# Kernel optimization log

Measured on AMD Instinct MI355X. Metric: run time of the kernel, lower is better.

Reference implementation:

```python
import jax, jax.numpy as jnp
import numpy as np

LEVELS = [(100, 128), (50, 64), (25, 32), (13, 16), (7, 8)]
B, C, S = 16, 80, 17064  # batch, class_num, sum(h*w)
GAMMA, ALPHA = 2.0, 0.25


def setup_inputs() -> dict:
    key = jax.random.key(0)
    ks = iter(jax.random.split(key, 40))
    inp = {}
    for i, (h, w) in enumerate(LEVELS):
        inp[f"cls_p{i}"] = jax.random.normal(next(ks), (B, C, h, w), dtype=jnp.float32)
        inp[f"cnt_p{i}"] = jax.random.normal(next(ks), (B, 1, h, w), dtype=jnp.float32)
        inp[f"reg_p{i}"] = jax.random.uniform(next(ks), (B, 4, h, w), dtype=jnp.float32) * 8.0 + 0.1
    keep = jax.random.uniform(next(ks), (B, S, 1)) > 0.7
    cnt_val = jax.random.uniform(next(ks), (B, S, 1), dtype=jnp.float32)
    inp["cnt_targets"] = jnp.where(keep, cnt_val, -1.0)
    inp["reg_targets"] = jax.random.uniform(next(ks), (B, S, 4), dtype=jnp.float32) * 8.0 + 0.1
    inp["cls_targets"] = jax.random.randint(next(ks), (B, S, 1), 0, 81, dtype=jnp.int64)
    return inp


def _flatten_levels(preds, c):
    # each pred [B,c,h,w] -> [B,h*w,c]; concat over levels -> [B,S,c]
    return jnp.concatenate(
        [p.transpose(0, 2, 3, 1).reshape(p.shape[0], -1, c) for p in preds], axis=1)


def _fcos_loss(cls_ps, cnt_ps, reg_ps, cls_t, cnt_t, reg_t):
    mask = (cnt_t > -1.0)[..., 0]                       # [B,S] bool positive mask
    num_pos = jnp.clip(jnp.sum(mask, axis=1), 1).astype(jnp.float32)  # [B]

    # ---- focal cls loss (over ALL locations, as in the original) ----
    cls = _flatten_levels(cls_ps, C)                    # [B,S,C]
    onehot = (jnp.arange(1, C + 1)[None, None, :] == cls_t).astype(jnp.float32)
    p = jax.nn.sigmoid(cls)
    p_t = onehot * p + (1.0 - onehot) * (1.0 - p)
    alpha_f = onehot * ALPHA + (1.0 - onehot) * (1.0 - ALPHA)
    focal = -alpha_f * (1.0 - p_t) ** GAMMA * jnp.log(p_t)
    cls_loss = jnp.mean(jnp.sum(focal, axis=(1, 2)) / num_pos)

    # ---- centerness BCE-with-logits, masked sum ----
    cnt = _flatten_levels(cnt_ps, 1)[..., 0]            # [B,S]
    t = cnt_t[..., 0]
    bce = jnp.maximum(cnt, 0.0) - cnt * t + jnp.log1p(jnp.exp(-jnp.abs(cnt)))
    cnt_loss = jnp.mean(jnp.sum(bce * mask, axis=1) / num_pos)

    # ---- GIoU reg loss, masked sum ----
    reg = _flatten_levels(reg_ps, 4)                    # [B,S,4] ltrb offsets
    lt_min = jnp.minimum(reg[..., :2], reg_t[..., :2])
    rb_min = jnp.minimum(reg[..., 2:], reg_t[..., 2:])
    wh_min = jnp.clip(rb_min + lt_min, 0.0)
    overlap = wh_min[..., 0] * wh_min[..., 1]
    area1 = (reg[..., 2] + reg[..., 0]) * (reg[..., 3] + reg[..., 1])
    area2 = (reg_t[..., 2] + reg_t[..., 0]) * (reg_t[..., 3] + reg_t[..., 1])
    union = area1 + area2 - overlap
    iou = overlap / union
    lt_max = jnp.maximum(reg[..., :2], reg_t[..., :2])
    rb_max = jnp.maximum(reg[..., 2:], reg_t[..., 2:])
    wh_max = jnp.clip(rb_max + lt_max, 0.0)
    g_area = wh_max[..., 0] * wh_max[..., 1]
    giou = iou - (g_area - union) / jnp.clip(g_area, 1e-10)
    reg_loss = jnp.mean(jnp.sum((1.0 - giou) * mask, axis=1) / num_pos)

    total = cls_loss + cnt_loss + reg_loss  # add_centerness=True
    return (cls_loss, cnt_loss, reg_loss, total)


def reference(cls_p0, cls_p1, cls_p2, cls_p3, cls_p4,
              cnt_p0, cnt_p1, cnt_p2, cnt_p3, cnt_p4,
              reg_p0, reg_p1, reg_p2, reg_p3, reg_p4,
              cnt_targets, reg_targets, cls_targets):
    return _fcos_loss([cls_p0, cls_p1, cls_p2, cls_p3, cls_p4],
                      [cnt_p0, cnt_p1, cnt_p2, cnt_p3, cnt_p4],
                      [reg_p0, reg_p1, reg_p2, reg_p3, reg_p4],
                      cls_targets, cnt_targets, reg_targets)
```

## Files before the change

### kernel.cpp

```cpp
#include <hip/hip_runtime.h>

#define S_TOTAL 17064
#define NB 16
#define NC 80
#define QPB 4266
#define NXQ 17

#define NA_BLOCKS 2064
#define SLOTS_PER_B 129
#define WSB 2064
#define NBXQ (NB * NXQ)

typedef float vfloat4 __attribute__((ext_vector_type(4)));

struct Ptrs {
    const float* cls[5];
    const float* cnt[5];
    const float* reg[5];
    const float* cnt_t;
    const float* reg_t;
    const int*   cls_t;
    float*       ws;
    float*       out;
};

__device__ __forceinline__ float focal_term(float x, bool o) {
    const float xs = o ? x : -x;
    const float af = o ? 0.25f : 0.75f;
    const float em = __expf(-xs);
    const float pt = 1.0f / (1.0f + em);
    const float q  = em * pt;
    return af * q * q * __logf(1.0f + em);
}

__device__ __forceinline__ float giou_term(float pl, float pt_, float pr, float pb,
                                           float tl, float tt, float tr, float tb) {
    const float overlap = fmaxf(fminf(pr, tr) + fminf(pl, tl), 0.0f) *
                          fmaxf(fminf(pb, tb) + fminf(pt_, tt), 0.0f);
    const float area1 = (pr + pl) * (pb + pt_);
    const float area2 = (tr + tl) * (tb + tt);
    const float uni = area1 + area2 - overlap;
    const float iou = overlap / uni;
    const float ga = fmaxf(fmaxf(pr, tr) + fmaxf(pl, tl), 0.0f) *
                     fmaxf(fmaxf(pb, tb) + fmaxf(pt_, tt), 0.0f);
    const float giou = iou - (ga - uni) / fmaxf(ga, 1e-10f);
    return 1.0f - giou;
}

__device__ __forceinline__ float bce_term(float x, float t) {
    return fmaxf(x, 0.0f) - x * t + __logf(1.0f + __expf(-fabsf(x)));
}

__global__ __launch_bounds__(256) void fcos_neg(Ptrs p) {
    const int bx = (int)blockIdx.x;

    int lvl, b, cnk, slot, CH, TOT;
    if (bx < 1536)      { lvl = 0; b = bx / 96;  cnk = bx - 96 * b;
                          slot = cnk;        CH = 2667; TOT = 256000; }
    else if (bx < 1920) { const int r = bx - 1536; lvl = 1; b = r / 24; cnk = r - 24 * b;
                          slot = 96 + cnk;   CH = 2667; TOT = 64000; }
    else if (bx < 2016) { const int r = bx - 1920; lvl = 2; b = r / 6;  cnk = r - 6 * b;
                          slot = 120 + cnk;  CH = 2667; TOT = 16000; }
    else if (bx < 2048) { const int r = bx - 2016; lvl = 3; b = r >> 1; cnk = r & 1;
                          slot = 126 + cnk;  CH = 2080; TOT = 4160; }
    else                { const int r = bx - 2048; lvl = 4; b = r;      cnk = 0;
                          slot = 128;        CH = 1120; TOT = 1120; }

    const vfloat4* bp = (const vfloat4*)(p.cls[lvl] + (size_t)b * 4 * TOT);
    const int i0   = cnk * CH;
    const int iend = min(i0 + CH, TOT);

    float acc = 0.f;
    #pragma unroll 2
    for (int i = i0 + (int)threadIdx.x; i < iend; i += 256) {
        const vfloat4 v = bp[i];
        acc += (focal_term(v.x, false) + focal_term(v.y, false)) +
               (focal_term(v.z, false) + focal_term(v.w, false));
    }

    #pragma unroll
    for (int d = 32; d; d >>= 1) acc += __shfl_down(acc, d);

    __shared__ float red[4];
    const int wave = threadIdx.x >> 6;
    if ((threadIdx.x & 63) == 0) red[wave] = acc;
    __syncthreads();
    if (threadIdx.x == 0)
        p.ws[b * SLOTS_PER_B + slot] = (red[0] + red[1]) + (red[2] + red[3]);
}

__global__ __launch_bounds__(256) void fcos_pos(Ptrs p) {
    const int bid = (int)blockIdx.x;
    const int b   = bid / NXQ;
    const int xq  = bid - b * NXQ;
    const int fq  = xq * 256 + (int)threadIdx.x;

    int lvl, qb, hw, off;
    if (fq < 3200)      { lvl = 0; qb = 0;    hw = 12800; off = 0;     }
    else if (fq < 4000) { lvl = 1; qb = 3200; hw = 3200;  off = 12800; }
    else if (fq < 4200) { lvl = 2; qb = 4000; hw = 800;   off = 16000; }
    else if (fq < 4252) { lvl = 3; qb = 4200; hw = 208;   off = 16800; }
    else                { lvl = 4; qb = 4252; hw = 56;    off = 17008; }
    const bool active = (fq < QPB);

    float corr = 0.f, acnt = 0.f, areg = 0.f, apos = 0.f;

    if (active) {
        const int s0  = (fq - qb) << 2;
        const int gs0 = b * S_TOTAL + off + s0;
        const int4 tq = *(const int4*)(p.cls_t + gs0);
        const float* cb = p.cls[lvl] + (size_t)(b * NC) * hw + s0;

        #pragma unroll
        for (int e = 0; e < 4; ++e) {
            const int ti = (e == 0) ? tq.x : (e == 1) ? tq.y : (e == 2) ? tq.z : tq.w;
            if (ti > 0) {
                const float x = cb[(size_t)(ti - 1) * hw + e];
                corr += focal_term(x, true) - focal_term(x, false);
            }
        }

        const float4 tC  = *(const float4*)(p.cnt_t + gs0);
        const float4 xc  = *(const float4*)(p.cnt[lvl] + (size_t)(b * hw + s0));
        const float m0 = (tC.x > -1.0f) ? 1.0f : 0.0f;
        const float m1 = (tC.y > -1.0f) ? 1.0f : 0.0f;
        const float m2 = (tC.z > -1.0f) ? 1.0f : 0.0f;
        const float m3 = (tC.w > -1.0f) ? 1.0f : 0.0f;
        apos = m0 + m1 + m2 + m3;
        acnt = bce_term(xc.x, tC.x) * m0 + bce_term(xc.y, tC.y) * m1 +
               bce_term(xc.z, tC.z) * m2 + bce_term(xc.w, tC.w) * m3;

        const float* rp  = p.reg[lvl] + (size_t)(b * 4 * hw + s0);
        const float4 pl  = *(const float4*)(rp);
        const float4 pt_ = *(const float4*)(rp + (size_t)hw);
        const float4 pr  = *(const float4*)(rp + (size_t)(2 * hw));
        const float4 pb  = *(const float4*)(rp + (size_t)(3 * hw));
        const float4 t0  = *(const float4*)(p.reg_t + (size_t)(gs0 + 0) * 4);
        const float4 t1  = *(const float4*)(p.reg_t + (size_t)(gs0 + 1) * 4);
        const float4 t2  = *(const float4*)(p.reg_t + (size_t)(gs0 + 2) * 4);
        const float4 t3  = *(const float4*)(p.reg_t + (size_t)(gs0 + 3) * 4);

        areg = giou_term(pl.x, pt_.x, pr.x, pb.x, t0.x, t0.y, t0.z, t0.w) * m0 +
               giou_term(pl.y, pt_.y, pr.y, pb.y, t1.x, t1.y, t1.z, t1.w) * m1 +
               giou_term(pl.z, pt_.z, pr.z, pb.z, t2.x, t2.y, t2.z, t2.w) * m2 +
               giou_term(pl.w, pt_.w, pr.w, pb.w, t3.x, t3.y, t3.z, t3.w) * m3;
    }

    #pragma unroll
    for (int d = 32; d; d >>= 1) {
        corr += __shfl_down(corr, d);
        acnt += __shfl_down(acnt, d);
        areg += __shfl_down(areg, d);
        apos += __shfl_down(apos, d);
    }

    __shared__ float red[4][4];
    const int wave = threadIdx.x >> 6;
    const int lane = threadIdx.x & 63;
    if (lane == 0) {
        red[0][wave] = corr; red[1][wave] = acnt;
        red[2][wave] = areg; red[3][wave] = apos;
    }
    __syncthreads();
    if (threadIdx.x == 0) {
        const int s = b * NXQ + xq;
        p.ws[WSB + 0 * NBXQ + s] = red[0][0] + red[0][1] + red[0][2] + red[0][3];
        p.ws[WSB + 1 * NBXQ + s] = red[1][0] + red[1][1] + red[1][2] + red[1][3];
        p.ws[WSB + 2 * NBXQ + s] = red[2][0] + red[2][1] + red[2][2] + red[2][3];
        p.ws[WSB + 3 * NBXQ + s] = red[3][0] + red[3][1] + red[3][2] + red[3][3];
    }
}

__global__ __launch_bounds__(256) void fcos_finalize(const float* __restrict__ ws,
                                                     float* __restrict__ out) {
    __shared__ float s[4][256];
    __shared__ float lb[3][NB];
    const int t = (int)threadIdx.x;
    const int b = t >> 4;
    const int k = t & 15;

    float qc = 0.f;
    for (int i = k; i < SLOTS_PER_B; i += 16) qc += ws[b * SLOTS_PER_B + i];
    float q1 = 0.f, q2 = 0.f, q3 = 0.f;
    for (int i = k; i < NXQ; i += 16) {
        const int sl = b * NXQ + i;
        qc += ws[WSB + 0 * NBXQ + sl];
        q1 += ws[WSB + 1 * NBXQ + sl];
        q2 += ws[WSB + 2 * NBXQ + sl];
        q3 += ws[WSB + 3 * NBXQ + sl];
    }
    s[0][t] = qc; s[1][t] = q1; s[2][t] = q2; s[3][t] = q3;
    __syncthreads();

    if (t < NB) {
        float cls = 0.f, cnt = 0.f, reg = 0.f, pos = 0.f;
        #pragma unroll
        for (int kk = 0; kk < 16; ++kk) {
            cls += s[0][t * 16 + kk];
            cnt += s[1][t * 16 + kk];
            reg += s[2][t * 16 + kk];
            pos += s[3][t * 16 + kk];
        }
        const float np = fmaxf(pos, 1.0f);
        lb[0][t] = cls / np;
        lb[1][t] = cnt / np;
        lb[2][t] = reg / np;
    }
    __syncthreads();

    if (t == 0) {
        float l0 = 0.f, l1 = 0.f, l2 = 0.f;
        #pragma unroll
        for (int bb = 0; bb < NB; ++bb) {
            l0 += lb[0][bb]; l1 += lb[1][bb]; l2 += lb[2][bb];
        }
        l0 *= (1.0f / NB); l1 *= (1.0f / NB); l2 *= (1.0f / NB);
        out[0] = l0;
        out[1] = l1;
        out[2] = l2;
        out[3] = l0 + l1 + l2;
    }
}

extern "C" void kernel_launch(void* const* d_in, const int* in_sizes, int n_in,
                              void* d_out, int out_size, void* d_ws, size_t ws_size,
                              hipStream_t stream) {
    Ptrs p;
    for (int i = 0; i < 5; ++i) {
        p.cls[i] = (const float*)d_in[3 * i + 0];
        p.cnt[i] = (const float*)d_in[3 * i + 1];
        p.reg[i] = (const float*)d_in[3 * i + 2];
    }
    p.cnt_t = (const float*)d_in[15];
    p.reg_t = (const float*)d_in[16];
    p.cls_t = (const int*)  d_in[17];
    p.ws    = (float*)d_ws;
    p.out   = (float*)d_out;

    fcos_neg<<<dim3(NA_BLOCKS), 256, 0, stream>>>(p);
    fcos_pos<<<dim3(NBXQ), 256, 0, stream>>>(p);
    fcos_finalize<<<dim3(1), 256, 0, stream>>>((const float*)d_ws, (float*)d_out);
}
```

Before: 161.3 us.

## Merge negative and positive passes into one kernel with per-element target labels

The separate negative-sweep and positive-correction kernels become a single launch that branches on block index. The cls sweep now reads the class-target row for each element and computes the exact focal term with the right one-hot flag, so the scattered gather-based correction is gone. One launch and one dependent global gather are removed, at the cost of extra int4 target loads and an integer division per vector in the hot loop, plus a templated loop structure.

After: 153.5 us. -4.9%, faster.

```diff
diff --git a/kernel.cpp b/kernel.cpp
--- a/kernel.cpp
+++ b/kernel.cpp
@@ -10,6 +10,7 @@
 #define SLOTS_PER_B 129
 #define WSB 2064
 #define NBXQ (NB * NXQ)
+#define TOTAL_GRID (NA_BLOCKS + NBXQ)
 
 typedef float vfloat4 __attribute__((ext_vector_type(4)));
 
@@ -51,123 +52,136 @@
     return fmaxf(x, 0.0f) - x * t + __logf(1.0f + __expf(-fabsf(x)));
 }
 
-__global__ __launch_bounds__(256) void fcos_neg(Ptrs p) {
+__device__ __forceinline__ float focal_quad(vfloat4 v, int4 t, int c1) {
+    return (focal_term(v.x, t.x == c1) + focal_term(v.y, t.y == c1)) +
+           (focal_term(v.z, t.z == c1) + focal_term(v.w, t.w == c1));
+}
+
+template <int HW4>
+__device__ __forceinline__ float sweep_cls(const vfloat4* __restrict__ bp,
+                                           const int* __restrict__ ct,
+                                           int u0, int stride) {
+    const int SPAN = NC * HW4;
+    float a0 = 0.f, a1 = 0.f;
+    int u = u0;
+    for (; u + stride < SPAN; u += 2 * stride) {
+        const int ub = u + stride;
+        const vfloat4 va = bp[u];
+        const vfloat4 vb = bp[ub];
+        const int ca = u / HW4;
+        const int cb = ub / HW4;
+        const int4 ta = *(const int4*)(ct + ((u  - ca * HW4) << 2));
+        const int4 tb = *(const int4*)(ct + ((ub - cb * HW4) << 2));
+        a0 += focal_quad(va, ta, ca + 1);
+        a1 += focal_quad(vb, tb, cb + 1);
+    }
+    if (u < SPAN) {
+        const vfloat4 v = bp[u];
+        const int c = u / HW4;
+        const int4 t = *(const int4*)(ct + ((u - c * HW4) << 2));
+        a0 += focal_quad(v, t, c + 1);
+    }
+    return a0 + a1;
+}
+
+__global__ __launch_bounds__(256) void fcos_main(Ptrs p) {
     const int bx = (int)blockIdx.x;
-
-    int lvl, b, cnk, slot, CH, TOT;
-    if (bx < 1536)      { lvl = 0; b = bx / 96;  cnk = bx - 96 * b;
-                          slot = cnk;        CH = 2667; TOT = 256000; }
-    else if (bx < 1920) { const int r = bx - 1536; lvl = 1; b = r / 24; cnk = r - 24 * b;
-                          slot = 96 + cnk;   CH = 2667; TOT = 64000; }
-    else if (bx < 2016) { const int r = bx - 1920; lvl = 2; b = r / 6;  cnk = r - 6 * b;
-                          slot = 120 + cnk;  CH = 2667; TOT = 16000; }
-    else if (bx < 2048) { const int r = bx - 2016; lvl = 3; b = r >> 1; cnk = r & 1;
-                          slot = 126 + cnk;  CH = 2080; TOT = 4160; }
-    else                { const int r = bx - 2048; lvl = 4; b = r;      cnk = 0;
-                          slot = 128;        CH = 1120; TOT = 1120; }
-
-    const vfloat4* bp = (const vfloat4*)(p.cls[lvl] + (size_t)b * 4 * TOT);
-    const int i0   = cnk * CH;
-    const int iend = min(i0 + CH, TOT);
-
-    float acc = 0.f;
-    #pragma unroll 2
-    for (int i = i0 + (int)threadIdx.x; i < iend; i += 256) {
-        const vfloat4 v = bp[i];
-        acc += (focal_term(v.x, false) + focal_term(v.y, false)) +
-               (focal_term(v.z, false) + focal_term(v.w, false));
-    }
-
-    #pragma unroll
-    for (int d = 32; d; d >>= 1) acc += __shfl_down(acc, d);
-
-    __shared__ float red[4];
-    const int wave = threadIdx.x >> 6;
-    if ((threadIdx.x & 63) == 0) red[wave] = acc;
-    __syncthreads();
-    if (threadIdx.x == 0)
-        p.ws[b * SLOTS_PER_B + slot] = (red[0] + red[1]) + (red[2] + red[3]);
-}
-
-__global__ __launch_bounds__(256) void fcos_pos(Ptrs p) {
-    const int bid = (int)blockIdx.x;
-    const int b   = bid / NXQ;
-    const int xq  = bid - b * NXQ;
-    const int fq  = xq * 256 + (int)threadIdx.x;
-
-    int lvl, qb, hw, off;
-    if (fq < 3200)      { lvl = 0; qb = 0;    hw = 12800; off = 0;     }
-    else if (fq < 4000) { lvl = 1; qb = 3200; hw = 3200;  off = 12800; }
-    else if (fq < 4200) { lvl = 2; qb = 4000; hw = 800;   off = 16000; }
-    else if (fq < 4252) { lvl = 3; qb = 4200; hw = 208;   off = 16800; }
-    else                { lvl = 4; qb = 4252; hw = 56;    off = 17008; }
-    const bool active = (fq < QPB);
-
-    float corr = 0.f, acnt = 0.f, areg = 0.f, apos = 0.f;
-
-    if (active) {
-        const int s0  = (fq - qb) << 2;
-        const int gs0 = b * S_TOTAL + off + s0;
-        const int4 tq = *(const int4*)(p.cls_t + gs0);
-        const float* cb = p.cls[lvl] + (size_t)(b * NC) * hw + s0;
-
-        #pragma unroll
-        for (int e = 0; e < 4; ++e) {
-            const int ti = (e == 0) ? tq.x : (e == 1) ? tq.y : (e == 2) ? tq.z : tq.w;
-            if (ti > 0) {
-                const float x = cb[(size_t)(ti - 1) * hw + e];
-                corr += focal_term(x, true) - focal_term(x, false);
-            }
-        }
-
-        const float4 tC  = *(const float4*)(p.cnt_t + gs0);
-        const float4 xc  = *(const float4*)(p.cnt[lvl] + (size_t)(b * hw + s0));
-        const float m0 = (tC.x > -1.0f) ? 1.0f : 0.0f;
-        const float m1 = (tC.y > -1.0f) ? 1.0f : 0.0f;
-        const float m2 = (tC.z > -1.0f) ? 1.0f : 0.0f;
-        const float m3 = (tC.w > -1.0f) ? 1.0f : 0.0f;
-        apos = m0 + m1 + m2 + m3;
-        acnt = bce_term(xc.x, tC.x) * m0 + bce_term(xc.y, tC.y) * m1 +
-               bce_term(xc.z, tC.z) * m2 + bce_term(xc.w, tC.w) * m3;
-
-        const float* rp  = p.reg[lvl] + (size_t)(b * 4 * hw + s0);
-        const float4 pl  = *(const float4*)(rp);
-        const float4 pt_ = *(const float4*)(rp + (size_t)hw);
-        const float4 pr  = *(const float4*)(rp + (size_t)(2 * hw));
-        const float4 pb  = *(const float4*)(rp + (size_t)(3 * hw));
-        const float4 t0  = *(const float4*)(p.reg_t + (size_t)(gs0 + 0) * 4);
-        const float4 t1  = *(const float4*)(p.reg_t + (size_t)(gs0 + 1) * 4);
-        const float4 t2  = *(const float4*)(p.reg_t + (size_t)(gs0 + 2) * 4);
-        const float4 t3  = *(const float4*)(p.reg_t + (size_t)(gs0 + 3) * 4);
-
-        areg = giou_term(pl.x, pt_.x, pr.x, pb.x, t0.x, t0.y, t0.z, t0.w) * m0 +
-               giou_term(pl.y, pt_.y, pr.y, pb.y, t1.x, t1.y, t1.z, t1.w) * m1 +
-               giou_term(pl.z, pt_.z, pr.z, pb.z, t2.x, t2.y, t2.z, t2.w) * m2 +
-               giou_term(pl.w, pt_.w, pr.w, pb.w, t3.x, t3.y, t3.z, t3.w) * m3;
-    }
-
-    #pragma unroll
-    for (int d = 32; d; d >>= 1) {
-        corr += __shfl_down(corr, d);
-        acnt += __shfl_down(acnt, d);
-        areg += __shfl_down(areg, d);
-        apos += __shfl_down(apos, d);
-    }
-
     __shared__ float red[4][4];
     const int wave = threadIdx.x >> 6;
     const int lane = threadIdx.x & 63;
-    if (lane == 0) {
-        red[0][wave] = corr; red[1][wave] = acnt;
-        red[2][wave] = areg; red[3][wave] = apos;
-    }
-    __syncthreads();
-    if (threadIdx.x == 0) {
-        const int s = b * NXQ + xq;
-        p.ws[WSB + 0 * NBXQ + s] = red[0][0] + red[0][1] + red[0][2] + red[0][3];
-        p.ws[WSB + 1 * NBXQ + s] = red[1][0] + red[1][1] + red[1][2] + red[1][3];
-        p.ws[WSB + 2 * NBXQ + s] = red[2][0] + red[2][1] + red[2][2] + red[2][3];
-        p.ws[WSB + 3 * NBXQ + s] = red[3][0] + red[3][1] + red[3][2] + red[3][3];
+
+    if (bx < NA_BLOCKS) {
+        int lvl, b, cnk, Kb, slot;
+        if (bx < 1536)      { lvl = 0; b = bx / 96;  cnk = bx - 96 * b;  Kb = 96; slot = cnk; }
+        else if (bx < 1920) { const int r = bx - 1536; lvl = 1; b = r / 24; cnk = r - 24 * b; Kb = 24; slot = 96 + cnk; }
+        else if (bx < 2016) { const int r = bx - 1920; lvl = 2; b = r / 6;  cnk = r - 6 * b;  Kb = 6;  slot = 120 + cnk; }
+        else if (bx < 2048) { const int r = bx - 2016; lvl = 3; b = r >> 1; cnk = r & 1;      Kb = 2;  slot = 126 + cnk; }
+        else                { lvl = 4; b = bx - 2048;  cnk = 0;            Kb = 1;            slot = 128; }
+
+        const int u0     = cnk * 256 + (int)threadIdx.x;
+        const int stride = Kb * 256;
+        float acc = 0.f;
+        switch (lvl) {
+            case 0: acc = sweep_cls<3200>((const vfloat4*)p.cls[0] + (size_t)b * (NC * 3200),
+                                          p.cls_t + b * S_TOTAL + 0,     u0, stride); break;
+            case 1: acc = sweep_cls<800>((const vfloat4*)p.cls[1] + (size_t)b * (NC * 800),
+                                          p.cls_t + b * S_TOTAL + 12800, u0, stride); break;
+            case 2: acc = sweep_cls<200>((const vfloat4*)p.cls[2] + (size_t)b * (NC * 200),
+                                          p.cls_t + b * S_TOTAL + 16000, u0, stride); break;
+            case 3: acc = sweep_cls<52>((const vfloat4*)p.cls[3] + (size_t)b * (NC * 52),
+                                          p.cls_t + b * S_TOTAL + 16800, u0, stride); break;
+            default: acc = sweep_cls<14>((const vfloat4*)p.cls[4] + (size_t)b * (NC * 14),
+                                          p.cls_t + b * S_TOTAL + 17008, u0, stride); break;
+        }
+
+        #pragma unroll
+        for (int d = 32; d; d >>= 1) acc += __shfl_down(acc, d);
+        if (lane == 0) red[0][wave] = acc;
+        __syncthreads();
+        if (threadIdx.x == 0)
+            p.ws[b * SLOTS_PER_B + slot] = (red[0][0] + red[0][1]) + (red[0][2] + red[0][3]);
+
+    } else {
+        const int bid = bx - NA_BLOCKS;
+        const int b   = bid / NXQ;
+        const int xq  = bid - b * NXQ;
+        const int fq  = xq * 256 + (int)threadIdx.x;
+
+        int lvl, qb, hw, off;
+        if (fq < 3200)      { lvl = 0; qb = 0;    hw = 12800; off = 0;     }
+        else if (fq < 4000) { lvl = 1; qb = 3200; hw = 3200;  off = 12800; }
+        else if (fq < 4200) { lvl = 2; qb = 4000; hw = 800;   off = 16000; }
+        else if (fq < 4252) { lvl = 3; qb = 4200; hw = 208;   off = 16800; }
+        else                { lvl = 4; qb = 4252; hw = 56;    off = 17008; }
+        const bool active = (fq < QPB);
+
+        float acnt = 0.f, areg = 0.f, apos = 0.f;
+        if (active) {
+            const int s0  = (fq - qb) << 2;
+            const int gs0 = b * S_TOTAL + off + s0;
+            const float4 tC  = *(const float4*)(p.cnt_t + gs0);
+            const float4 xc  = *(const float4*)(p.cnt[lvl] + (size_t)(b * hw + s0));
+            const float m0 = (tC.x > -1.0f) ? 1.0f : 0.0f;
+            const float m1 = (tC.y > -1.0f) ? 1.0f : 0.0f;
+            const float m2 = (tC.z > -1.0f) ? 1.0f : 0.0f;
+            const float m3 = (tC.w > -1.0f) ? 1.0f : 0.0f;
+            apos = m0 + m1 + m2 + m3;
+            acnt = bce_term(xc.x, tC.x) * m0 + bce_term(xc.y, tC.y) * m1 +
+                   bce_term(xc.z, tC.z) * m2 + bce_term(xc.w, tC.w) * m3;
+
+            const float* rp  = p.reg[lvl] + (size_t)(b * 4 * hw + s0);
+            const float4 pl  = *(const float4*)(rp);
+            const float4 pt_ = *(const float4*)(rp + (size_t)hw);
+            const float4 pr  = *(const float4*)(rp + (size_t)(2 * hw));
+            const float4 pb  = *(const float4*)(rp + (size_t)(3 * hw));
+            const float4 t0  = *(const float4*)(p.reg_t + (size_t)(gs0 + 0) * 4);
+            const float4 t1  = *(const float4*)(p.reg_t + (size_t)(gs0 + 1) * 4);
+            const float4 t2  = *(const float4*)(p.reg_t + (size_t)(gs0 + 2) * 4);
+            const float4 t3  = *(const float4*)(p.reg_t + (size_t)(gs0 + 3) * 4);
+
+            areg = giou_term(pl.x, pt_.x, pr.x, pb.x, t0.x, t0.y, t0.z, t0.w) * m0 +
+                   giou_term(pl.y, pt_.y, pr.y, pb.y, t1.x, t1.y, t1.z, t1.w) * m1 +
+                   giou_term(pl.z, pt_.z, pr.z, pb.z, t2.x, t2.y, t2.z, t2.w) * m2 +
+                   giou_term(pl.w, pt_.w, pr.w, pb.w, t3.x, t3.y, t3.z, t3.w) * m3;
+        }
+
+        #pragma unroll
+        for (int d = 32; d; d >>= 1) {
+            acnt += __shfl_down(acnt, d);
+            areg += __shfl_down(areg, d);
+            apos += __shfl_down(apos, d);
+        }
+        if (lane == 0) {
+            red[1][wave] = acnt; red[2][wave] = areg; red[3][wave] = apos;
+        }
+        __syncthreads();
+        if (threadIdx.x == 0) {
+            const int s = b * NXQ + xq;
+            p.ws[WSB + 0 * NBXQ + s] = 0.0f;
+            p.ws[WSB + 1 * NBXQ + s] = red[1][0] + red[1][1] + red[1][2] + red[1][3];
+            p.ws[WSB + 2 * NBXQ + s] = red[2][0] + red[2][1] + red[2][2] + red[2][3];
+            p.ws[WSB + 3 * NBXQ + s] = red[3][0] + red[3][1] + red[3][2] + red[3][3];
+        }
     }
 }
 
@@ -237,7 +251,6 @@
     p.ws    = (float*)d_ws;
     p.out   = (float*)d_out;
 
-    fcos_neg<<<dim3(NA_BLOCKS), 256, 0, stream>>>(p);
-    fcos_pos<<<dim3(NBXQ), 256, 0, stream>>>(p);
+    fcos_main<<<dim3(TOTAL_GRID), 256, 0, stream>>>(p);
     fcos_finalize<<<dim3(1), 256, 0, stream>>>((const float*)d_ws, (float*)d_out);
 }
```
